# Kernel optimization log

Hardware: AMD Instinct MI355X
Metric: run time of the kernel (lower is better)

The kernel has to match this reference:

```python
import jax, jax.numpy as jnp
import numpy as np

N_HEADS = 16
HEAD_SIZE = 128  # n_embd // n_vq_heads = 2048 // 16
N_OPTIONS = 512


def setup_inputs() -> dict:
    key = jax.random.key(0)
    k1, k2, k3 = jax.random.split(key, 3)
    B, S, E = 4, 2048, N_HEADS * HEAD_SIZE
    x = jax.random.normal(k1, (B, S, E), dtype=jnp.float32)
    vq_head_weights = jax.random.normal(k2, (N_HEADS, N_OPTIONS, HEAD_SIZE), dtype=jnp.float32)
    vq_codebooks = jax.random.normal(k3, (N_HEADS, N_OPTIONS, HEAD_SIZE), dtype=jnp.float32)
    temperature = jnp.float32(1.0)
    return {
        "x": x,
        "vq_head_weights": vq_head_weights,
        "vq_codebooks": vq_codebooks,
        "temperature": temperature,
    }


def reference(x, vq_head_weights, vq_codebooks, temperature):
    # Training-mode forward of VQizer (softmax path).
    B, S, E = x.shape
    H, O, A = vq_head_weights.shape  # heads, options, head_size
    x_prepped = x.reshape(B, S, H, A)
    # per-head logits over codebook options
    logits = jnp.einsum('bsha,hoa->bsho', x_prepped, vq_head_weights)
    probs = jax.nn.softmax(logits / temperature, axis=-1)
    out = jnp.einsum('bsho,hoa->bsha', probs, vq_codebooks)
    return out.reshape(B, S, H * A)
```

## Files before the change

kernel.cpp:

```cpp
#include <hip/hip_runtime.h>
#include <math.h>

#define NHEADS 16
#define HS     128
#define NOPT   512
#define TB     128
#define OC     32
#define NCH    16
#define EMB    2048
#define LOG2E  1.44269504088896340736f
#define THRD   11.0f

typedef short bf16x8 __attribute__((ext_vector_type(8)));
typedef _Float16 f16x8 __attribute__((ext_vector_type(8)));
typedef unsigned short u16x8 __attribute__((ext_vector_type(8)));
typedef float f32x4 __attribute__((ext_vector_type(4)));
typedef float f32x16 __attribute__((ext_vector_type(16)));
typedef unsigned u32x4 __attribute__((ext_vector_type(4)));

__device__ __forceinline__ unsigned short f2bf(float f) {
    union { float f; unsigned u; } v; v.f = f;
    unsigned r = v.u + 0x7FFFu + ((v.u >> 16) & 1u);
    return (unsigned short)(r >> 16);
}
__device__ __forceinline__ float bf2f(unsigned short h) {
    union { unsigned u; float f; } v; v.u = ((unsigned)h) << 16;
    return v.f;
}
__device__ __forceinline__ unsigned short f2h(float f) {
    const _Float16 h = (_Float16)f;
    return __builtin_bit_cast(unsigned short, h);
}
__device__ __forceinline__ void gll16(const void* gptr, void* lptr) {
    __builtin_amdgcn_global_load_lds(
        (const __attribute__((address_space(1))) void*)gptr,
        (__attribute__((address_space(3))) void*)lptr,
        16, 0, 0);
}
__device__ __forceinline__ unsigned pkrtz(float lo, float hi) {
    unsigned r;
    asm("v_cvt_pkrtz_f16_f32 %0, %1, %2" : "=v"(r) : "v"(lo), "v"(hi));
    return r;
}
__device__ __forceinline__ void pl32swap(unsigned &a, unsigned &b) {
    asm volatile("v_permlane32_swap_b32 %0, %1" : "+v"(a), "+v"(b));
}
__device__ __forceinline__ f32x16 mfma32h(f16x8 a, f16x8 b, f32x16 c) {
    return __builtin_amdgcn_mfma_f32_32x32x16_f16(a, b, c, 0, 0, 0);
}

#define WCH    4096
#define CCH    4096
#define WS_C0  (NHEADS * NCH * WCH)
#define WS_TOTAL_BYTES ((size_t)(WS_C0 + NHEADS * NCH * CCH) * 2)

__global__ __launch_bounds__(256) void vq_prep(const float* __restrict__ W,
                                               const float* __restrict__ C,
                                               const float* __restrict__ temp,
                                               unsigned short* __restrict__ ws)
{
    const int b = blockIdx.x, t = threadIdx.x;
    if (b < NHEADS * NCH) {
        const float scW = (1.0f / temp[0]) * LOG2E;
        const float* src = W + (size_t)b * OC * HS;
        unsigned short* dst = ws + (size_t)b * WCH;
        for (int k = 0; k < 16; ++k) {
            const int e = k * 256 + t;
            const int opt = e >> 7, col = e & 127;
            dst[opt * 128 + (col ^ ((opt & 15) << 3))] = f2h(src[e] * scW);
        }
    } else {
        const int b2 = b - NHEADS * NCH;
        const float* src = C + (size_t)b2 * OC * HS;
        unsigned short* dst = ws + WS_C0 + (size_t)b2 * CCH;
        for (int k = 0; k < 16; ++k) {
            const int e = k * 256 + t;
            const int opt = e >> 7, a = e & 127;
            dst[a * 32 + (opt ^ (((a >> 1) & 3) << 3))] = f2h(src[e]);
        }
    }
}

__global__ __launch_bounds__(256, 3) void vq_main(
    const float* __restrict__ x, const unsigned short* __restrict__ ws,
    float* __restrict__ out)
{
    __shared__ unsigned short wbuf[3][WCH];
    __shared__ unsigned short cbuf[3][CCH];

    const int t = threadIdx.x, l = t & 63, w = t >> 6;
    const int la = l & 31, hf = l >> 5;
    const int b = blockIdx.x;
    const int head = ((b & 7) << 1) | ((b >> 3) & 1);
    const int n0 = (b >> 4) * TB;

    const unsigned short* gwbase = ws + (size_t)(head * NCH) * WCH;
    const unsigned short* gcbase = ws + WS_C0 + (size_t)(head * NCH) * CCH;

    f16x8 xf[8];
    {
        const float* xr = x + (size_t)(n0 + w * 32 + la) * EMB + head * HS + hf * 8;
        #pragma unroll
        for (int kb = 0; kb < 8; ++kb) {
            const float4 v0 = *(const float4*)(xr + kb * 16);
            const float4 v1 = *(const float4*)(xr + kb * 16 + 4);
            const float vv[8] = {v0.x, v0.y, v0.z, v0.w, v1.x, v1.y, v1.z, v1.w};
            u16x8 hh;
            #pragma unroll
            for (int j = 0; j < 8; ++j) hh[j] = f2h(vv[j]);
            xf[kb] = __builtin_bit_cast(f16x8, hh);
        }
    }

    #pragma unroll
    for (int p = 0; p < 2; ++p) {
        const char* gw = (const char*)(gwbase + (size_t)p * WCH) + w * 2048 + l * 16;
        char* lw = (char*)&wbuf[p][0] + w * 2048;
        gll16(gw, lw); gll16(gw + 1024, lw + 1024);
        const char* gc = (const char*)(gcbase + (size_t)p * CCH) + w * 2048 + l * 16;
        char* lc = (char*)&cbuf[p][0] + w * 2048;
        gll16(gc, lc); gll16(gc + 1024, lc + 1024);
    }

    f32x16 O0 = (f32x16)0.0f, O1 = (f32x16)0.0f, O2 = (f32x16)0.0f, O3 = (f32x16)0.0f;
    float M = -1.0e30f, sacc = 0.0f;

    asm volatile("s_waitcnt vmcnt(4)" ::: "memory");
    __builtin_amdgcn_s_barrier();

    int bc = 0;
    for (int c = 0; c < NCH; ++c) {
        if (c + 2 < NCH) {
            int bp = bc + 2; if (bp >= 3) bp -= 3;
            const char* gw = (const char*)(gwbase + (size_t)(c + 2) * WCH) + w * 2048 + l * 16;
            char* lw = (char*)&wbuf[bp][0] + w * 2048;
            gll16(gw, lw); gll16(gw + 1024, lw + 1024);
            const char* gc = (const char*)(gcbase + (size_t)(c + 2) * CCH) + w * 2048 + l * 16;
            char* lc = (char*)&cbuf[bp][0] + w * 2048;
            gll16(gc, lc); gll16(gc + 1024, lc + 1024);
        }

        f32x16 sa = (f32x16)0.0f, sb = (f32x16)0.0f;
        const unsigned short* wb = &wbuf[bc][0];
        #pragma unroll
        for (int kb = 0; kb < 8; ++kb) {
            const int idx = la * 128 + ((kb * 16 + hf * 8) ^ ((la & 15) << 3));
            const f16x8 wf = *(const f16x8*)&wb[idx];
            if (kb & 1) sb = mfma32h(wf, xf[kb], sb);
            else        sa = mfma32h(wf, xf[kb], sa);
        }
        const f32x16 S = sa + sb;

        float m8[8];
        #pragma unroll
        for (int i = 0; i < 8; ++i) m8[i] = fmaxf(S[2 * i], S[2 * i + 1]);
        float m4a = fmaxf(m8[0], m8[1]), m4b = fmaxf(m8[2], m8[3]);
        float m4c = fmaxf(m8[4], m8[5]), m4d = fmaxf(m8[6], m8[7]);
        float cmax = fmaxf(fmaxf(m4a, m4b), fmaxf(m4c, m4d));
        cmax = fmaxf(cmax, __shfl_xor(cmax, 32));
        if (__any(cmax > M + THRD)) {
            const float Mn = fmaxf(M, cmax);
            const float fr = exp2f(M - Mn);
            M = Mn;
            sacc *= fr;
            #pragma unroll
            for (int q = 0; q < 16; ++q) {
                const int row = (q & 3) + 8 * (q >> 2) + 4 * hf;
                const float f = __shfl(fr, row);
                O0[q] *= f; O1[q] *= f; O2[q] *= f; O3[q] *= f;
            }
        }
        float pv[16];
        #pragma unroll
        for (int q = 0; q < 16; ++q) pv[q] = exp2f(S[q] - M);
        {
            float s8[8];
            #pragma unroll
            for (int i = 0; i < 8; ++i) s8[i] = pv[2 * i] + pv[2 * i + 1];
            sacc += ((s8[0] + s8[1]) + (s8[2] + s8[3])) +
                    ((s8[4] + s8[5]) + (s8[6] + s8[7]));
        }

        unsigned pk0 = pkrtz(pv[0],  pv[1]),  pk1 = pkrtz(pv[2],  pv[3]);
        unsigned pk2 = pkrtz(pv[4],  pv[5]),  pk3 = pkrtz(pv[6],  pv[7]);
        unsigned pk4 = pkrtz(pv[8],  pv[9]),  pk5 = pkrtz(pv[10], pv[11]);
        unsigned pk6 = pkrtz(pv[12], pv[13]), pk7 = pkrtz(pv[14], pv[15]);
        pl32swap(pk0, pk2);
        pl32swap(pk1, pk3);
        pl32swap(pk4, pk6);
        pl32swap(pk5, pk7);
        const f16x8 pa0 = __builtin_bit_cast(f16x8, (u32x4){pk0, pk1, pk2, pk3});
        const f16x8 pa1 = __builtin_bit_cast(f16x8, (u32x4){pk4, pk5, pk6, pk7});

        const unsigned short* cb = &cbuf[bc][0];
        {
            const int a0 = la;
            const int sw0 = ((a0 >> 1) & 3) << 3;
            O0 = mfma32h(pa0, *(const f16x8*)&cb[a0 * 32 + ((hf * 8) ^ sw0)], O0);
            O0 = mfma32h(pa1, *(const f16x8*)&cb[a0 * 32 + ((16 + hf * 8) ^ sw0)], O0);
            const int a1 = 32 + la;
            const int sw1 = ((a1 >> 1) & 3) << 3;
            O1 = mfma32h(pa0, *(const f16x8*)&cb[a1 * 32 + ((hf * 8) ^ sw1)], O1);
            O1 = mfma32h(pa1, *(const f16x8*)&cb[a1 * 32 + ((16 + hf * 8) ^ sw1)], O1);
            const int a2 = 64 + la;
            const int sw2 = ((a2 >> 1) & 3) << 3;
            O2 = mfma32h(pa0, *(const f16x8*)&cb[a2 * 32 + ((hf * 8) ^ sw2)], O2);
            O2 = mfma32h(pa1, *(const f16x8*)&cb[a2 * 32 + ((16 + hf * 8) ^ sw2)], O2);
            const int a3 = 96 + la;
            const int sw3 = ((a3 >> 1) & 3) << 3;
            O3 = mfma32h(pa0, *(const f16x8*)&cb[a3 * 32 + ((hf * 8) ^ sw3)], O3);
            O3 = mfma32h(pa1, *(const f16x8*)&cb[a3 * 32 + ((16 + hf * 8) ^ sw3)], O3);
        }

        if (c < NCH - 2) { asm volatile("s_waitcnt vmcnt(4)" ::: "memory"); }
        else             { asm volatile("s_waitcnt vmcnt(0)" ::: "memory"); }
        __builtin_amdgcn_s_barrier();
        ++bc; if (bc >= 3) bc -= 3;
    }

    const float stot = sacc + __shfl_xor(sacc, 32);
    const float rs = 1.0f / stot;
    #pragma unroll
    for (int q = 0; q < 16; ++q) {
        const int row = (q & 3) + 8 * (q >> 2) + 4 * hf;
        const float rq = __shfl(rs, row);
        float* op = out + (size_t)(n0 + w * 32 + row) * EMB + head * HS + la;
        op[0]  = O0[q] * rq;
        op[32] = O1[q] * rq;
        op[64] = O2[q] * rq;
        op[96] = O3[q] * rq;
    }
}

__global__ __launch_bounds__(256, 2) void vq_fwd_mfma(
    const float* __restrict__ x, const float* __restrict__ W,
    const float* __restrict__ C, const float* __restrict__ temp,
    float* __restrict__ out)
{
    __shared__ unsigned short xh_lds[64 * HS];
    __shared__ unsigned short xl_lds[64 * HS];
    __shared__ unsigned short wst[2][64 * HS];
    __shared__ unsigned short p_lds[4][16 * 64];

    const int t = threadIdx.x, l = t & 63, w = t >> 6, lr = l & 15, lk = l >> 4;
    const int b = blockIdx.x;
    const int h = ((b & 7) << 1) | ((b >> 3) & 1);
    const int n0 = (b >> 4) * 64;
    const float invT = 1.0f / temp[0];

    #pragma unroll
    for (int kk = 0; kk < 4; ++kk) {
        const int g = t + 256 * kk;
        const int row = g >> 4, c8 = (g & 15) * 8;
        const float* src = x + (size_t)(n0 + row) * EMB + h * HS + c8;
        const float4 v0 = *(const float4*)src;
        const float4 v1 = *(const float4*)(src + 4);
        float vv[8] = {v0.x, v0.y, v0.z, v0.w, v1.x, v1.y, v1.z, v1.w};
        u16x8 hh, ll;
        #pragma unroll
        for (int j = 0; j < 8; ++j) {
            const unsigned short hb = f2bf(vv[j]);
            hh[j] = hb; ll[j] = f2bf(vv[j] - bf2f(hb));
        }
        const int idx = row * HS + (c8 ^ ((row & 7) << 3));
        *(u16x8*)&xh_lds[idx] = hh;
        *(u16x8*)&xl_lds[idx] = ll;
    }

    f32x4 acc[32];
    #pragma unroll
    for (int i = 0; i < 32; ++i) acc[i] = f32x4{0.f, 0.f, 0.f, 0.f};
    bf16x8 axh[4], axl[4];

    #pragma unroll
    for (int c = 0; c < 8; ++c) {
        if (c) __syncthreads();
        #pragma unroll
        for (int kk = 0; kk < 4; ++kk) {
            const int g = t + 256 * kk;
            const int row = g >> 4, c8 = (g & 15) * 8;
            const float* src = W + ((size_t)h * NOPT + c * 64 + row) * HS + c8;
            const float4 v0 = *(const float4*)src;
            const float4 v1 = *(const float4*)(src + 4);
            float vv[8] = {v0.x, v0.y, v0.z, v0.w, v1.x, v1.y, v1.z, v1.w};
            u16x8 hh, ll;
            #pragma unroll
            for (int j = 0; j < 8; ++j) {
                const unsigned short hb = f2bf(vv[j]);
                hh[j] = hb; ll[j] = f2bf(vv[j] - bf2f(hb));
            }
            const int idx = row * HS + (c8 ^ ((row & 7) << 3));
            *(u16x8*)&wst[0][idx] = hh;
            *(u16x8*)&wst[1][idx] = ll;
        }
        __syncthreads();
        if (c == 0) {
            const int arow = w * 16 + lr;
            #pragma unroll
            for (int ks = 0; ks < 4; ++ks) {
                const int ai = arow * HS + ((lk * 8 + ks * 32) ^ ((arow & 7) << 3));
                axh[ks] = *(const bf16x8*)&xh_lds[ai];
                axl[ks] = *(const bf16x8*)&xl_lds[ai];
            }
        }
        #pragma unroll
        for (int nt = 0; nt < 4; ++nt) {
            const int brow = nt * 16 + lr;
            #pragma unroll
            for (int ks = 0; ks < 4; ++ks) {
                const int bi = brow * HS + ((lk * 8 + ks * 32) ^ ((brow & 7) << 3));
                const bf16x8 bh = *(const bf16x8*)&wst[0][bi];
                const bf16x8 bl = *(const bf16x8*)&wst[1][bi];
                acc[c*4+nt] = __builtin_amdgcn_mfma_f32_16x16x32_bf16(axh[ks], bh, acc[c*4+nt], 0, 0, 0);
                acc[c*4+nt] = __builtin_amdgcn_mfma_f32_16x16x32_bf16(axl[ks], bh, acc[c*4+nt], 0, 0, 0);
                acc[c*4+nt] = __builtin_amdgcn_mfma_f32_16x16x32_bf16(axh[ks], bl, acc[c*4+nt], 0, 0, 0);
            }
        }
    }

    float mx[4], rsn[4];
    #pragma unroll
    for (int r = 0; r < 4; ++r) {
        float m = -3.0e38f;
        #pragma unroll
        for (int i = 0; i < 32; ++i) m = fmaxf(m, acc[i][r]);
        m *= invT;
        #pragma unroll
        for (int s = 1; s < 16; s <<= 1) m = fmaxf(m, __shfl_xor(m, s));
        float sum = 0.f;
        #pragma unroll
        for (int i = 0; i < 32; ++i) sum += exp2f((acc[i][r] * invT - m) * LOG2E);
        #pragma unroll
        for (int s = 1; s < 16; s <<= 1) sum += __shfl_xor(sum, s);
        mx[r] = m; rsn[r] = 1.0f / sum;
    }

    f32x4 oacc[8];
    #pragma unroll
    for (int i = 0; i < 8; ++i) oacc[i] = f32x4{0.f, 0.f, 0.f, 0.f};
    const int pr_ = t & 31, ag = t >> 5;
    #pragma unroll
    for (int c = 0; c < 8; ++c) {
        __syncthreads();
        {
            const float* c0p = C + ((size_t)h * NOPT + c * 64 + 2 * pr_) * HS + ag * 16;
            float va[16], vb[16];
            #pragma unroll
            for (int q = 0; q < 4; ++q) {
                const float4 u0 = ((const float4*)c0p)[q];
                const float4 u1 = ((const float4*)(c0p + HS))[q];
                va[q*4+0] = u0.x; va[q*4+1] = u0.y; va[q*4+2] = u0.z; va[q*4+3] = u0.w;
                vb[q*4+0] = u1.x; vb[q*4+1] = u1.y; vb[q*4+2] = u1.z; vb[q*4+3] = u1.w;
            }
            unsigned* ct32 = (unsigned*)&wst[0][0];
            #pragma unroll
            for (int j = 0; j < 16; ++j) {
                const int a = ag * 16 + j;
                const unsigned pkv = (unsigned)f2bf(va[j]) | ((unsigned)f2bf(vb[j]) << 16);
                ct32[a * 32 + (pr_ ^ ((a & 7) << 2))] = pkv;
            }
        }
        #pragma unroll
        for (int nt = 0; nt < 4; ++nt) {
            #pragma unroll
            for (int r = 0; r < 4; ++r) {
                const float p = exp2f((acc[c*4+nt][r] * invT - mx[r]) * LOG2E);
                const int prow = lk * 4 + r;
                const int pcol = nt * 16 + lr;
                p_lds[w][prow * 64 + (pcol ^ ((prow & 7) << 3))] = f2bf(p);
            }
        }
        __syncthreads();
        #pragma unroll
        for (int ks = 0; ks < 2; ++ks) {
            const int ai = lr * 64 + ((lk * 8 + ks * 32) ^ ((lr & 7) << 3));
            const bf16x8 pa = *(const bf16x8*)&p_lds[w][ai];
            #pragma unroll
            for (int nt = 0; nt < 8; ++nt) {
                const int brow = nt * 16 + lr;
                const int bi = brow * 64 + ((lk * 8 + ks * 32) ^ ((brow & 7) << 3));
                const bf16x8 cbv = *(const bf16x8*)&wst[0][bi];
                oacc[nt] = __builtin_amdgcn_mfma_f32_16x16x32_bf16(pa, cbv, oacc[nt], 0, 0, 0);
            }
        }
    }

    #pragma unroll
    for (int nt = 0; nt < 8; ++nt) {
        #pragma unroll
        for (int r = 0; r < 4; ++r) {
            const int tok = n0 + w * 16 + lk * 4 + r;
            out[(size_t)tok * EMB + h * HS + nt * 16 + lr] = oacc[nt][r] * rsn[r];
        }
    }
}

extern "C" void kernel_launch(void* const* d_in, const int* in_sizes, int n_in,
                              void* d_out, int out_size, void* d_ws, size_t ws_size,
                              hipStream_t stream) {
    const float* x = (const float*)d_in[0];
    const float* W = (const float*)d_in[1];
    const float* C = (const float*)d_in[2];
    const float* T = (const float*)d_in[3];
    float* out     = (float*)d_out;

    const int ntok = in_sizes[0] / EMB;

    if (ws_size >= WS_TOTAL_BYTES) {
        hipLaunchKernelGGL(vq_prep, dim3(NHEADS * NCH * 2), dim3(256), 0, stream,
                           W, C, T, (unsigned short*)d_ws);
        const int nblk = (ntok / TB) * NHEADS;
        hipLaunchKernelGGL(vq_main, dim3(nblk), dim3(256), 0, stream,
                           x, (const unsigned short*)d_ws, out);
    } else {
        const int nblk = (ntok / 64) * NHEADS;
        hipLaunchKernelGGL(vq_fwd_mfma, dim3(nblk), dim3(256), 0, stream,
                           x, W, C, T, out);
    }
}
```

Before: 78.89 us.

## Switch to double-buffered LDS and raise occupancy to four blocks per CU

Drops the triple-buffered codebook/weight staging (prefetch distance two) in favour of double buffering with prefetch distance one. This cuts LDS per block and raises launch bounds from three to four waves per SIMD. It also issues the first chunk's loads before the x conversion, uses a single MFMA accumulator instead of two, and reuses the score registers for the exponentials to save VGPRs. The trade-off is less load-latency hiding per block, since each iteration now waits for all outstanding loads, in exchange for more resident blocks.

New measurement: 99.69 us. 1.26x slower.

```diff
diff --git a/kernel.cpp b/kernel.cpp
--- a/kernel.cpp
+++ b/kernel.cpp
@@ -81,12 +81,12 @@
     }
 }
 
-__global__ __launch_bounds__(256, 3) void vq_main(
+__global__ __launch_bounds__(256, 4) void vq_main(
     const float* __restrict__ x, const unsigned short* __restrict__ ws,
     float* __restrict__ out)
 {
-    __shared__ unsigned short wbuf[3][WCH];
-    __shared__ unsigned short cbuf[3][CCH];
+    __shared__ unsigned short wbuf[2][WCH];
+    __shared__ unsigned short cbuf[2][CCH];
 
     const int t = threadIdx.x, l = t & 63, w = t >> 6;
     const int la = l & 31, hf = l >> 5;
@@ -97,6 +97,15 @@
     const unsigned short* gwbase = ws + (size_t)(head * NCH) * WCH;
     const unsigned short* gcbase = ws + WS_C0 + (size_t)(head * NCH) * CCH;
 
+    {
+        const char* gw = (const char*)gwbase + w * 1024 + l * 16;
+        gll16(gw, (char*)&wbuf[0][0] + w * 1024);
+        const char* gc = (const char*)gcbase + w * 1024 + l * 16;
+        gll16(gc, (char*)&cbuf[0][0] + w * 1024);
+        gll16(gw + 4096, (char*)&wbuf[0][0] + 4096 + w * 1024);
+        gll16(gc + 4096, (char*)&cbuf[0][0] + 4096 + w * 1024);
+    }
+
     f16x8 xf[8];
     {
         const float* xr = x + (size_t)(n0 + w * 32 + la) * EMB + head * HS + hf * 8;
@@ -112,51 +121,34 @@
         }
     }
 
-    #pragma unroll
-    for (int p = 0; p < 2; ++p) {
-        const char* gw = (const char*)(gwbase + (size_t)p * WCH) + w * 2048 + l * 16;
-        char* lw = (char*)&wbuf[p][0] + w * 2048;
-        gll16(gw, lw); gll16(gw + 1024, lw + 1024);
-        const char* gc = (const char*)(gcbase + (size_t)p * CCH) + w * 2048 + l * 16;
-        char* lc = (char*)&cbuf[p][0] + w * 2048;
-        gll16(gc, lc); gll16(gc + 1024, lc + 1024);
-    }
-
     f32x16 O0 = (f32x16)0.0f, O1 = (f32x16)0.0f, O2 = (f32x16)0.0f, O3 = (f32x16)0.0f;
     float M = -1.0e30f, sacc = 0.0f;
 
-    asm volatile("s_waitcnt vmcnt(4)" ::: "memory");
+    asm volatile("s_waitcnt vmcnt(0)" ::: "memory");
     __builtin_amdgcn_s_barrier();
 
-    int bc = 0;
     for (int c = 0; c < NCH; ++c) {
-        if (c + 2 < NCH) {
-            int bp = bc + 2; if (bp >= 3) bp -= 3;
-            const char* gw = (const char*)(gwbase + (size_t)(c + 2) * WCH) + w * 2048 + l * 16;
-            char* lw = (char*)&wbuf[bp][0] + w * 2048;
-            gll16(gw, lw); gll16(gw + 1024, lw + 1024);
-            const char* gc = (const char*)(gcbase + (size_t)(c + 2) * CCH) + w * 2048 + l * 16;
-            char* lc = (char*)&cbuf[bp][0] + w * 2048;
-            gll16(gc, lc); gll16(gc + 1024, lc + 1024);
-        }
-
-        f32x16 sa = (f32x16)0.0f, sb = (f32x16)0.0f;
-        const unsigned short* wb = &wbuf[bc][0];
+        const int cur = c & 1;
+        if (c + 1 < NCH) {
+            const char* gw = (const char*)(gwbase + (size_t)(c + 1) * WCH) + w * 1024 + l * 16;
+            char* lw = (char*)&wbuf[cur ^ 1][0] + w * 1024;
+            gll16(gw, lw); gll16(gw + 4096, lw + 4096);
+            const char* gc = (const char*)(gcbase + (size_t)(c + 1) * CCH) + w * 1024 + l * 16;
+            char* lc = (char*)&cbuf[cur ^ 1][0] + w * 1024;
+            gll16(gc, lc); gll16(gc + 4096, lc + 4096);
+        }
+
+        f32x16 S = (f32x16)0.0f;
+        const unsigned short* wb = &wbuf[cur][0];
         #pragma unroll
         for (int kb = 0; kb < 8; ++kb) {
             const int idx = la * 128 + ((kb * 16 + hf * 8) ^ ((la & 15) << 3));
-            const f16x8 wf = *(const f16x8*)&wb[idx];
-            if (kb & 1) sb = mfma32h(wf, xf[kb], sb);
-            else        sa = mfma32h(wf, xf[kb], sa);
-        }
-        const f32x16 S = sa + sb;
-
-        float m8[8];
-        #pragma unroll
-        for (int i = 0; i < 8; ++i) m8[i] = fmaxf(S[2 * i], S[2 * i + 1]);
-        float m4a = fmaxf(m8[0], m8[1]), m4b = fmaxf(m8[2], m8[3]);
-        float m4c = fmaxf(m8[4], m8[5]), m4d = fmaxf(m8[6], m8[7]);
-        float cmax = fmaxf(fmaxf(m4a, m4b), fmaxf(m4c, m4d));
+            S = mfma32h(*(const f16x8*)&wb[idx], xf[kb], S);
+        }
+
+        float cmax = fmaxf(S[0], S[1]);
+        #pragma unroll
+        for (int i = 2; i < 16; i += 2) cmax = fmaxf(fmaxf(cmax, S[i]), S[i + 1]);
         cmax = fmaxf(cmax, __shfl_xor(cmax, 32));
         if (__any(cmax > M + THRD)) {
             const float Mn = fmaxf(M, cmax);
@@ -170,21 +162,20 @@
                 O0[q] *= f; O1[q] *= f; O2[q] *= f; O3[q] *= f;
             }
         }
-        float pv[16];
-        #pragma unroll
-        for (int q = 0; q < 16; ++q) pv[q] = exp2f(S[q] - M);
+        #pragma unroll
+        for (int q = 0; q < 16; ++q) S[q] = exp2f(S[q] - M);
         {
             float s8[8];
             #pragma unroll
-            for (int i = 0; i < 8; ++i) s8[i] = pv[2 * i] + pv[2 * i + 1];
+            for (int i = 0; i < 8; ++i) s8[i] = S[2 * i] + S[2 * i + 1];
             sacc += ((s8[0] + s8[1]) + (s8[2] + s8[3])) +
                     ((s8[4] + s8[5]) + (s8[6] + s8[7]));
         }
 
-        unsigned pk0 = pkrtz(pv[0],  pv[1]),  pk1 = pkrtz(pv[2],  pv[3]);
-        unsigned pk2 = pkrtz(pv[4],  pv[5]),  pk3 = pkrtz(pv[6],  pv[7]);
-        unsigned pk4 = pkrtz(pv[8],  pv[9]),  pk5 = pkrtz(pv[10], pv[11]);
-        unsigned pk6 = pkrtz(pv[12], pv[13]), pk7 = pkrtz(pv[14], pv[15]);
+        unsigned pk0 = pkrtz(S[0],  S[1]),  pk1 = pkrtz(S[2],  S[3]);
+        unsigned pk2 = pkrtz(S[4],  S[5]),  pk3 = pkrtz(S[6],  S[7]);
+        unsigned pk4 = pkrtz(S[8],  S[9]),  pk5 = pkrtz(S[10], S[11]);
+        unsigned pk6 = pkrtz(S[12], S[13]), pk7 = pkrtz(S[14], S[15]);
         pl32swap(pk0, pk2);
         pl32swap(pk1, pk3);
         pl32swap(pk4, pk6);
@@ -192,7 +183,7 @@
         const f16x8 pa0 = __builtin_bit_cast(f16x8, (u32x4){pk0, pk1, pk2, pk3});
         const f16x8 pa1 = __builtin_bit_cast(f16x8, (u32x4){pk4, pk5, pk6, pk7});
 
-        const unsigned short* cb = &cbuf[bc][0];
+        const unsigned short* cb = &cbuf[cur][0];
         {
             const int a0 = la;
             const int sw0 = ((a0 >> 1) & 3) << 3;
@@ -212,10 +203,8 @@
             O3 = mfma32h(pa1, *(const f16x8*)&cb[a3 * 32 + ((16 + hf * 8) ^ sw3)], O3);
         }
 
-        if (c < NCH - 2) { asm volatile("s_waitcnt vmcnt(4)" ::: "memory"); }
-        else             { asm volatile("s_waitcnt vmcnt(0)" ::: "memory"); }
-        __builtin_amdgcn_s_barrier();
-        ++bc; if (bc >= 3) bc -= 3;
+        asm volatile("s_waitcnt vmcnt(0)" ::: "memory");
+        if (c + 1 < NCH) __builtin_amdgcn_s_barrier();
     }
 
     const float stot = sacc + __shfl_xor(sacc, 32);
```
